# Kernel optimization log

Measured on AMD Instinct MI355X. Metric: run time of the kernel, lower is better.

Reference implementation:

```python
import jax, jax.numpy as jnp
import numpy as np

B, N, E, F, FE = 4, 10000, 160000, 128, 16  # batch, nodes, edges, filters(=node feat dim), edge feat dim
EPS = 1e-3  # keras LayerNormalization default epsilon


def layernorm(x, gamma, beta):
    mu = jnp.mean(x, axis=-1, keepdims=True)
    var = jnp.mean(jnp.square(x - mu), axis=-1, keepdims=True)
    return (x - mu) * jax.lax.rsqrt(var + EPS) * gamma + beta


def setup_inputs() -> dict:
    key = jax.random.key(0)
    ks = jax.random.split(key, 8)
    nodes = jax.random.normal(ks[0], (B, N, F), dtype=jnp.float32)
    edge_features = jax.random.normal(ks[1], (B, E, FE), dtype=jnp.float32)
    edges = jax.random.randint(ks[2], (B, E, 2), 0, N, dtype=jnp.int32)
    edge_weights = jax.random.uniform(ks[3], (B, E, 1), dtype=jnp.float32)
    edge_dropout = jnp.ones((B, E, 2), dtype=jnp.float32)
    W_msg = jax.random.normal(ks[4], (2 * F + FE, F), dtype=jnp.float32) * 0.02
    b_msg = jnp.zeros((F,), jnp.float32)
    g_msg = jnp.ones((F,), jnp.float32)
    beta_msg = jnp.zeros((F,), jnp.float32)
    W_upd = jax.random.normal(ks[5], (2 * F, F), dtype=jnp.float32) * 0.02
    b_upd = jnp.zeros((F,), jnp.float32)
    g_upd = jnp.ones((F,), jnp.float32)
    beta_upd = jnp.zeros((F,), jnp.float32)
    return dict(nodes=nodes, edge_features=edge_features, edges=edges,
                edge_weights=edge_weights, edge_dropout=edge_dropout,
                W_msg=W_msg, b_msg=b_msg, g_msg=g_msg, beta_msg=beta_msg,
                W_upd=W_upd, b_upd=b_upd, g_upd=g_upd, beta_upd=beta_upd)


def reference(nodes, edge_features, edges, edge_weights, edge_dropout,
              W_msg, b_msg, g_msg, beta_msg, W_upd, b_upd, g_upd, beta_upd):
    n = nodes.shape[1]
    # gather both endpoints per edge: [B,E,2,F] -> [B,E,2F]
    gathered = jax.vmap(lambda nd, ed: nd[ed])(nodes, edges)
    msg_in = gathered.reshape(gathered.shape[0], gathered.shape[1], -1)
    msg_in = jnp.concatenate([msg_in, edge_features], axis=-1)
    # message MLP: Dense + GELU + LayerNorm
    h = jnp.einsum('bei,io->beo', msg_in, W_msg) + b_msg
    messages = layernorm(jax.nn.gelu(h, approximate=False), g_msg, beta_msg)
    weighted_messages = messages * edge_weights
    # scatter-sum to destination nodes (edge[:,1]), masked by dropout col 1
    dropped = weighted_messages * edge_dropout[..., 1:2]
    dst = edges[..., 1]
    aggregated = jax.vmap(lambda m, d: jax.ops.segment_sum(m, d, num_segments=n))(dropped, dst)
    # update: concat + Dense + GELU + LayerNorm
    combined = jnp.concatenate([nodes, aggregated], axis=-1)
    u = jnp.einsum('bni,io->bno', combined, W_upd) + b_upd
    updated_nodes = layernorm(jax.nn.gelu(u, approximate=False), g_upd, beta_upd)
    return updated_nodes
```

## Files before the change

### kernel.cpp

```cpp
#include <hip/hip_runtime.h>
#include <hip/hip_bf16.h>
#include <hip/hip_fp16.h>

#define BATCH   4
#define NNODES  10000
#define NEDGES  160000
#define FDIM    128
#define FEDIM   16
#define LNEPS   1e-3f

typedef __attribute__((ext_vector_type(8))) short v8s;
typedef __attribute__((ext_vector_type(4))) float v4f;

#define AGG_BYTES   ((size_t)BATCH * NNODES * FDIM * 2)
#define P_OFF       AGG_BYTES
#define P_BYTES     ((size_t)BATCH * NNODES * 256 * 2)
#define WTCAT_OFF   (P_OFF + P_BYTES)
#define WTUPD_OFF   (WTCAT_OFF + (size_t)256 * 128 * 2)
#define W3T_OFF     (WTUPD_OFF + (size_t)128 * 256 * 2)

static __device__ __forceinline__ unsigned short f2bf(float f) {
    __hip_bfloat16 h = __float2bfloat16(f);
    return *reinterpret_cast<unsigned short*>(&h);
}
static __device__ __forceinline__ float bfbits2f(unsigned bits16) {
    return __uint_as_float(bits16 << 16);
}

static __device__ __forceinline__ float gelu_f(float x) {
    float z = 0.7978845608028654f * (x + 0.044715f * x * x * x);
    float e = __expf(2.0f * z);
    float t = 1.0f - 2.0f / (e + 1.0f);
    return 0.5f * x * (1.0f + t);
}

static __device__ __forceinline__ bool is_bf16_mode(const void* gflag) {
    return ((*reinterpret_cast<const unsigned*>(gflag)) & 0xFFFFu) != 0u;
}
static __device__ __forceinline__ float ld_f(const void* p, long i, bool bf) {
    return bf ? (float)reinterpret_cast<const __hip_bfloat16*>(p)[i]
              : reinterpret_cast<const float*>(p)[i];
}
static __device__ __forceinline__ uint4 pack8(const float* p) {
    float4 f0 = *reinterpret_cast<const float4*>(p);
    float4 f1 = *reinterpret_cast<const float4*>(p + 4);
    uint4 o;
    o.x = f2bf(f0.x) | ((unsigned)f2bf(f0.y) << 16);
    o.y = f2bf(f0.z) | ((unsigned)f2bf(f0.w) << 16);
    o.z = f2bf(f1.x) | ((unsigned)f2bf(f1.y) << 16);
    o.w = f2bf(f1.z) | ((unsigned)f2bf(f1.w) << 16);
    return o;
}
static __device__ __forceinline__ uint4 h8_to_bf8(uint4 u) {
    unsigned w[4] = {u.x, u.y, u.z, u.w};
    uint4 o; unsigned r[4];
    #pragma unroll
    for (int q = 0; q < 4; q++) {
        __half lo = *reinterpret_cast<const __half*>(&w[q]);
        unsigned short hib = (unsigned short)(w[q] >> 16);
        __half hi = *reinterpret_cast<const __half*>(&hib);
        r[q] = f2bf(__half2float(lo)) | ((unsigned)f2bf(__half2float(hi)) << 16);
    }
    o.x = r[0]; o.y = r[1]; o.z = r[2]; o.w = r[3];
    return o;
}

#define NCAT (256 * 128)
#define NUPD (128 * 256)
#define NW3  (128 * 32)
__global__ void prep_weights(const void* __restrict__ Wmsg, const void* __restrict__ Wupd,
                             const void* __restrict__ gflag,
                             unsigned short* __restrict__ WtCat,
                             unsigned short* __restrict__ WtUpd,
                             unsigned short* __restrict__ W3t) {
    bool bf = is_bf16_mode(gflag);
    int i = blockIdx.x * 256 + threadIdx.x;
    if (i < NCAT) {
        int n = i >> 7, k = i & 127;
        int src = (n < 128) ? (k * 128 + n) : ((128 + k) * 128 + (n - 128));
        WtCat[i] = bf ? reinterpret_cast<const unsigned short*>(Wmsg)[src]
                      : f2bf(reinterpret_cast<const float*>(Wmsg)[src]);
    } else if (i < NCAT + NUPD) {
        int j = i - NCAT;
        int n = j >> 8, c = j & 255;
        WtUpd[j] = bf ? reinterpret_cast<const unsigned short*>(Wupd)[c * 128 + n]
                      : f2bf(reinterpret_cast<const float*>(Wupd)[c * 128 + n]);
    } else if (i < NCAT + NUPD + NW3) {
        int j = i - NCAT - NUPD;
        int n = j >> 5, k = j & 31;
        W3t[j] = (k < 16) ? (bf ? reinterpret_cast<const unsigned short*>(Wmsg)[(256 + k) * 128 + n]
                                : f2bf(reinterpret_cast<const float*>(Wmsg)[(256 + k) * 128 + n]))
                          : (unsigned short)0;
    }
}

__global__ __launch_bounds__(256) void pg_kernel(
    const void* __restrict__ nodes,
    const void* __restrict__ bmsg,
    const void* __restrict__ gflag,
    const unsigned short* __restrict__ Wt,
    unsigned short*       __restrict__ P)
{
    const bool bf = is_bf16_mode(gflag);
    __shared__ unsigned short sW[128 * 40];
    __shared__ unsigned short sA[128 * 40];

    const int tid  = threadIdx.x;
    const int lane = tid & 63, wave = tid >> 6;
    const int c    = lane & 15, quad = lane >> 4;
    const int row0 = blockIdx.x * 128;
    const int half = blockIdx.y;
    const int NROWS = BATCH * NNODES;

    float bcol[8];
    #pragma unroll
    for (int nt = 0; nt < 8; nt++)
        bcol[nt] = (half == 0) ? ld_f(bmsg, nt * 16 + c, bf) : 0.f;

    v4f acc[2][8];
    #pragma unroll
    for (int mt = 0; mt < 2; mt++)
        #pragma unroll
        for (int nt = 0; nt < 8; nt++) { v4f z = {0.f, 0.f, 0.f, 0.f}; acc[mt][nt] = z; }

    for (int ks = 0; ks < 4; ks++) {
        #pragma unroll
        for (int q = tid; q < 512; q += 256) {
            int n = q >> 2, part = q & 3;
            *reinterpret_cast<uint4*>(&sW[n * 40 + part * 8]) =
                *reinterpret_cast<const uint4*>(Wt + (half * 128 + n) * 128 + ks * 32 + part * 8);
        }
        #pragma unroll
        for (int q = tid; q < 512; q += 256) {
            int t = q >> 2, part = q & 3;
            int row = row0 + t; if (row >= NROWS) row = NROWS - 1;
            long off = (size_t)row * FDIM + ks * 32 + part * 8;
            uint4 v = bf ? *reinterpret_cast<const uint4*>(reinterpret_cast<const unsigned short*>(nodes) + off)
                         : pack8(reinterpret_cast<const float*>(nodes) + off);
            *reinterpret_cast<uint4*>(&sA[t * 40 + part * 8]) = v;
        }
        __syncthreads();

        v8s a0 = *reinterpret_cast<const v8s*>(&sA[(wave * 32 + c) * 40 + quad * 8]);
        v8s a1 = *reinterpret_cast<const v8s*>(&sA[(wave * 32 + 16 + c) * 40 + quad * 8]);
        #pragma unroll
        for (int nt = 0; nt < 8; nt++) {
            v8s bfr = *reinterpret_cast<const v8s*>(&sW[(nt * 16 + c) * 40 + quad * 8]);
            acc[0][nt] = __builtin_amdgcn_mfma_f32_16x16x32_bf16(a0, bfr, acc[0][nt], 0, 0, 0);
            acc[1][nt] = __builtin_amdgcn_mfma_f32_16x16x32_bf16(a1, bfr, acc[1][nt], 0, 0, 0);
        }
        __syncthreads();
    }

    #pragma unroll
    for (int mt = 0; mt < 2; mt++)
        #pragma unroll
        for (int r = 0; r < 4; r++) {
            int row = row0 + wave * 32 + mt * 16 + quad * 4 + r;
            if (row < NROWS) {
                float v[8];
                #pragma unroll
                for (int nt = 0; nt < 8; nt++) v[nt] = acc[mt][nt][r] + bcol[nt];
                uint4 o;
                o.x = f2bf(v[0]) | ((unsigned)f2bf(v[1]) << 16);
                o.y = f2bf(v[2]) | ((unsigned)f2bf(v[3]) << 16);
                o.z = f2bf(v[4]) | ((unsigned)f2bf(v[5]) << 16);
                o.w = f2bf(v[6]) | ((unsigned)f2bf(v[7]) << 16);
                *reinterpret_cast<uint4*>(P + (size_t)row * 256 + half * 128 + c * 8) = o;
            }
        }
}

__global__ __launch_bounds__(256) void edge_kernel(
    const unsigned short* __restrict__ P,
    const void* __restrict__ efeat,
    const int*  __restrict__ edges,
    const void* __restrict__ ew,
    const void* __restrict__ ed,
    const unsigned short* __restrict__ W3t,
    const void* __restrict__ gmsg,
    const void* __restrict__ betamsg,
    __half*     __restrict__ agg)
{
    const bool bf = is_bf16_mode(gmsg);
    __shared__ int   sSrc[128], sDst[128];
    __shared__ float sWgt[128];

    const int tid  = threadIdx.x;
    const int b    = blockIdx.x / (NEDGES / 128);
    const int e0   = (blockIdx.x % (NEDGES / 128)) * 128;
    const int lane = tid & 63, wave = tid >> 6;
    const int c    = lane & 15, quad = lane >> 4;

    if (tid < 128) {
        long be = (long)b * NEDGES + e0 + tid;
        sSrc[tid] = edges[be * 2];
        sDst[tid] = edges[be * 2 + 1];
        sWgt[tid] = ld_f(ew, be, bf) * ld_f(ed, be * 2 + 1, bf);
    }

    float gcol[8], becol[8];
    #pragma unroll
    for (int nt = 0; nt < 8; nt++) {
        gcol[nt]  = ld_f(gmsg, nt * 16 + c, bf);
        becol[nt] = ld_f(betamsg, nt * 16 + c, bf);
    }

    v8s bfrag[8];
    #pragma unroll
    for (int nt = 0; nt < 8; nt++)
        bfrag[nt] = *reinterpret_cast<const v8s*>(W3t + (nt * 16 + c) * 32 + quad * 8);

    v4f acc[2][8];
    #pragma unroll
    for (int mt = 0; mt < 2; mt++)
        #pragma unroll
        for (int nt = 0; nt < 8; nt++) { v4f z = {0.f, 0.f, 0.f, 0.f}; acc[mt][nt] = z; }

    #pragma unroll
    for (int mt = 0; mt < 2; mt++) {
        v8s a = {0, 0, 0, 0, 0, 0, 0, 0};
        if (quad < 2) {
            long ebase = ((long)b * NEDGES + e0 + wave * 32 + mt * 16 + c) * FEDIM + quad * 8;
            if (bf) {
                uint4 u = *reinterpret_cast<const uint4*>(reinterpret_cast<const unsigned short*>(efeat) + ebase);
                a = *reinterpret_cast<v8s*>(&u);
            } else {
                uint4 u = pack8(reinterpret_cast<const float*>(efeat) + ebase);
                a = *reinterpret_cast<v8s*>(&u);
            }
        }
        #pragma unroll
        for (int nt = 0; nt < 8; nt++)
            acc[mt][nt] = __builtin_amdgcn_mfma_f32_16x16x32_bf16(a, bfrag[nt], acc[mt][nt], 0, 0, 0);
    }

    __syncthreads();

    const size_t nbase = (size_t)b * NNODES;
    const bool even = !(c & 1);

    #pragma unroll
    for (int mt = 0; mt < 2; mt++) {
        uint4 U1[4], U2[4];
        #pragma unroll
        for (int r = 0; r < 4; r++) {
            int m = wave * 32 + mt * 16 + quad * 4 + r;
            U1[r] = *reinterpret_cast<const uint4*>(P + (nbase + sSrc[m]) * 256 + c * 8);
            U2[r] = *reinterpret_cast<const uint4*>(P + (nbase + sDst[m]) * 256 + 128 + c * 8);
        }
        #pragma unroll
        for (int r = 0; r < 4; r++) {
            int m = wave * 32 + mt * 16 + quad * 4 + r;
            unsigned w1[4] = {U1[r].x, U1[r].y, U1[r].z, U1[r].w};
            unsigned w2[4] = {U2[r].x, U2[r].y, U2[r].z, U2[r].w};
            float h[8];
            #pragma unroll
            for (int q = 0; q < 4; q++) {
                h[q * 2]     = bfbits2f(w1[q] & 0xFFFFu) + bfbits2f(w2[q] & 0xFFFFu) + acc[mt][q * 2][r];
                h[q * 2 + 1] = __uint_as_float(w1[q] & 0xFFFF0000u) + __uint_as_float(w2[q] & 0xFFFF0000u)
                               + acc[mt][q * 2 + 1][r];
            }
            float s = 0.f, sq = 0.f;
            #pragma unroll
            for (int nt = 0; nt < 8; nt++) {
                float g = gelu_f(h[nt]);
                h[nt] = g; s += g; sq += g * g;
            }
            #pragma unroll
            for (int off = 1; off < 16; off <<= 1) {
                s  += __shfl_xor(s, off);
                sq += __shfl_xor(sq, off);
            }
            float mu  = s * (1.0f / 128.0f);
            float var = sq * (1.0f / 128.0f) - mu * mu;
            float rs  = rsqrtf(var + LNEPS);
            float wgt = sWgt[m];
            float y[8];
            #pragma unroll
            for (int nt = 0; nt < 8; nt++)
                y[nt] = ((h[nt] - mu) * rs * gcol[nt] + becol[nt]) * wgt;

            __half* aout = agg + (nbase + sDst[m]) * FDIM;
            #pragma unroll
            for (int np = 0; np < 4; np++) {
                int nt = np * 2;
                float t0 = __shfl_xor(y[nt], 1);
                float t1 = __shfl_xor(y[nt + 1], 1);
                __half2 v = even ? __floats2half2_rn(y[nt], t0)
                                 : __floats2half2_rn(t1, y[nt + 1]);
                int hoff = even ? (nt * 16 + c) : ((nt + 1) * 16 + c - 1);
                unsafeAtomicAdd(reinterpret_cast<__half2*>(aout + hoff), v);
            }
        }
    }
}

__global__ __launch_bounds__(256) void upd_kernel(
    const void* __restrict__ nodes,
    const __half* __restrict__ agg,
    const unsigned short* __restrict__ Wt,
    const void* __restrict__ bupd,
    const void* __restrict__ gupd,
    const void* __restrict__ beupd,
    void*       __restrict__ out)
{
    const bool bf = is_bf16_mode(gupd);
    __shared__ unsigned short sW[128 * 40];
    __shared__ unsigned short sA[64 * 40];

    const int tid  = threadIdx.x;
    const int lane = tid & 63, wave = tid >> 6;
    const int c    = lane & 15, quad = lane >> 4;
    const int row0 = blockIdx.x * 64;

    float bcol[8], gcol[8], becol[8];
    #pragma unroll
    for (int nt = 0; nt < 8; nt++) {
        int col = nt * 16 + c;
        bcol[nt]  = ld_f(bupd, col, bf);
        gcol[nt]  = ld_f(gupd, col, bf);
        becol[nt] = ld_f(beupd, col, bf);
    }

    v4f acc[8];
    #pragma unroll
    for (int nt = 0; nt < 8; nt++) { v4f z = {0.f, 0.f, 0.f, 0.f}; acc[nt] = z; }

    for (int ks = 0; ks < 8; ks++) {
        #pragma unroll
        for (int q = tid; q < 512; q += 256) {
            int n = q >> 2, part = q & 3;
            *reinterpret_cast<uint4*>(&sW[n * 40 + part * 8]) =
                *reinterpret_cast<const uint4*>(Wt + n * 256 + ks * 32 + part * 8);
        }
        {
            int t = tid >> 2, part = tid & 3;
            int row = row0 + t;
            uint4 v;
            if (ks < 4) {
                long off = (size_t)row * FDIM + ks * 32 + part * 8;
                v = bf ? *reinterpret_cast<const uint4*>(reinterpret_cast<const unsigned short*>(nodes) + off)
                       : pack8(reinterpret_cast<const float*>(nodes) + off);
            } else {
                uint4 u = *reinterpret_cast<const uint4*>(
                    reinterpret_cast<const unsigned short*>(agg) + (size_t)row * FDIM + (ks - 4) * 32 + part * 8);
                v = h8_to_bf8(u);
            }
            *reinterpret_cast<uint4*>(&sA[t * 40 + part * 8]) = v;
        }
        __syncthreads();

        v8s a0 = *reinterpret_cast<const v8s*>(&sA[(wave * 16 + c) * 40 + quad * 8]);
        #pragma unroll
        for (int nt = 0; nt < 8; nt++) {
            v8s bfr = *reinterpret_cast<const v8s*>(&sW[(nt * 16 + c) * 40 + quad * 8]);
            acc[nt] = __builtin_amdgcn_mfma_f32_16x16x32_bf16(a0, bfr, acc[nt], 0, 0, 0);
        }
        __syncthreads();
    }

    float s[4] = {0, 0, 0, 0}, sq[4] = {0, 0, 0, 0};
    #pragma unroll
    for (int nt = 0; nt < 8; nt++) {
        v4f v = acc[nt];
        #pragma unroll
        for (int r = 0; r < 4; r++) {
            float g = gelu_f(v[r] + bcol[nt]);
            v[r] = g;
            s[r] += g; sq[r] += g * g;
        }
        acc[nt] = v;
    }
    #pragma unroll
    for (int off = 1; off < 16; off <<= 1) {
        #pragma unroll
        for (int r = 0; r < 4; r++) {
            s[r]  += __shfl_xor(s[r], off);
            sq[r] += __shfl_xor(sq[r], off);
        }
    }
    #pragma unroll
    for (int r = 0; r < 4; r++) {
        float mu  = s[r] * (1.0f / 128.0f);
        float var = sq[r] * (1.0f / 128.0f) - mu * mu;
        float rs  = rsqrtf(var + LNEPS);
        int row = row0 + wave * 16 + quad * 4 + r;
        #pragma unroll
        for (int nt = 0; nt < 8; nt++) {
            float y = (acc[nt][r] - mu) * rs * gcol[nt] + becol[nt];
            size_t oi = (size_t)row * FDIM + nt * 16 + c;
            if (bf) reinterpret_cast<__hip_bfloat16*>(out)[oi] = __float2bfloat16(y);
            else    reinterpret_cast<float*>(out)[oi] = y;
        }
    }
}

extern "C" void kernel_launch(void* const* d_in, const int* in_sizes, int n_in,
                              void* d_out, int out_size, void* d_ws, size_t ws_size,
                              hipStream_t stream)
{
    const void* nodes   = d_in[0];
    const void* efeat   = d_in[1];
    const int*  edges   = (const int*)d_in[2];
    const void* ew      = d_in[3];
    const void* ed      = d_in[4];
    const void* Wmsg    = d_in[5];
    const void* bmsg    = d_in[6];
    const void* gmsg    = d_in[7];
    const void* betamsg = d_in[8];
    const void* Wupd    = d_in[9];
    const void* bupd    = d_in[10];
    const void* gupd    = d_in[11];
    const void* betaupd = d_in[12];

    char* ws = (char*)d_ws;
    __half* agg = (__half*)ws;
    unsigned short* P     = (unsigned short*)(ws + P_OFF);
    unsigned short* WtCat = (unsigned short*)(ws + WTCAT_OFF);
    unsigned short* WtUpd = (unsigned short*)(ws + WTUPD_OFF);
    unsigned short* W3t   = (unsigned short*)(ws + W3T_OFF);

    hipMemsetAsync(agg, 0, AGG_BYTES, stream);
    prep_weights<<<(NCAT + NUPD + NW3 + 255) / 256, 256, 0, stream>>>(
        Wmsg, Wupd, gmsg, WtCat, WtUpd, W3t);
    pg_kernel<<<dim3((BATCH * NNODES + 127) / 128, 2), 256, 0, stream>>>(
        nodes, bmsg, gmsg, WtCat, P);
    edge_kernel<<<BATCH * (NEDGES / 128), 256, 0, stream>>>(
        P, efeat, edges, ew, ed, W3t, gmsg, betamsg, agg);
    upd_kernel<<<BATCH * NNODES / 64, 256, 0, stream>>>(
        nodes, agg, WtUpd, bupd, gupd, betaupd, d_out);
}
```

Measured before the change: 291.0 us.

## Split update GEMM: precompute node half in pg_kernel, fp16 MFMA on agg

```diff
diff --git a/kernel.cpp b/kernel.cpp
--- a/kernel.cpp
+++ b/kernel.cpp
@@ -8,23 +8,35 @@
 #define FDIM    128
 #define FEDIM   16
 #define LNEPS   1e-3f
-
-typedef __attribute__((ext_vector_type(8))) short v8s;
-typedef __attribute__((ext_vector_type(4))) float v4f;
-
-#define AGG_BYTES   ((size_t)BATCH * NNODES * FDIM * 2)
+#define NROWS   (BATCH * NNODES)
+
+typedef __attribute__((ext_vector_type(8))) short    v8s;
+typedef _Float16 v8h __attribute__((ext_vector_type(8)));
+typedef __attribute__((ext_vector_type(4))) float    v4f;
+
+#define AGG_BYTES   ((size_t)NROWS * FDIM * 2)
 #define P_OFF       AGG_BYTES
-#define P_BYTES     ((size_t)BATCH * NNODES * 256 * 2)
-#define WTCAT_OFF   (P_OFF + P_BYTES)
-#define WTUPD_OFF   (WTCAT_OFF + (size_t)256 * 128 * 2)
-#define W3T_OFF     (WTUPD_OFF + (size_t)128 * 256 * 2)
+#define P_BYTES     ((size_t)NROWS * 256 * 2)
+#define P3_OFF      (P_OFF + P_BYTES)
+#define P3_BYTES    ((size_t)NROWS * 128 * 2)
+#define WTCAT_OFF   (P3_OFF + P3_BYTES)
+#define W3T_OFF     (WTCAT_OFF + (size_t)384 * 128 * 2)
+#define WU2F_OFF    (W3T_OFF + (size_t)128 * 32 * 2)
 
 static __device__ __forceinline__ unsigned short f2bf(float f) {
     __hip_bfloat16 h = __float2bfloat16(f);
     return *reinterpret_cast<unsigned short*>(&h);
 }
+static __device__ __forceinline__ unsigned short f2h(float f) {
+    __half h = __float2half(f);
+    return *reinterpret_cast<unsigned short*>(&h);
+}
 static __device__ __forceinline__ float bfbits2f(unsigned bits16) {
     return __uint_as_float(bits16 << 16);
+}
+static __device__ __forceinline__ float hbits2f(unsigned short b) {
+    __half h = *reinterpret_cast<const __half*>(&b);
+    return __half2float(h);
 }
 
 static __device__ __forceinline__ float gelu_f(float x) {
@@ -51,55 +63,44 @@
     o.w = f2bf(f1.z) | ((unsigned)f2bf(f1.w) << 16);
     return o;
 }
-static __device__ __forceinline__ uint4 h8_to_bf8(uint4 u) {
-    unsigned w[4] = {u.x, u.y, u.z, u.w};
-    uint4 o; unsigned r[4];
-    #pragma unroll
-    for (int q = 0; q < 4; q++) {
-        __half lo = *reinterpret_cast<const __half*>(&w[q]);
-        unsigned short hib = (unsigned short)(w[q] >> 16);
-        __half hi = *reinterpret_cast<const __half*>(&hib);
-        r[q] = f2bf(__half2float(lo)) | ((unsigned)f2bf(__half2float(hi)) << 16);
-    }
-    o.x = r[0]; o.y = r[1]; o.z = r[2]; o.w = r[3];
-    return o;
-}
-
-#define NCAT (256 * 128)
-#define NUPD (128 * 256)
+
+#define NCAT (384 * 128)
 #define NW3  (128 * 32)
-__global__ void prep_weights(const void* __restrict__ Wmsg, const void* __restrict__ Wupd,
-                             const void* __restrict__ gflag,
-                             unsigned short* __restrict__ WtCat,
-                             unsigned short* __restrict__ WtUpd,
-                             unsigned short* __restrict__ W3t) {
+#define NU2  (128 * 128)
+#define NZERO ((int)(AGG_BYTES / 16))
+__global__ void prep_kernel(const void* __restrict__ Wmsg, const void* __restrict__ Wupd,
+                            const void* __restrict__ gflag,
+                            unsigned short* __restrict__ WtCat,
+                            unsigned short* __restrict__ W3t,
+                            unsigned short* __restrict__ Wu2f,
+                            uint4* __restrict__ aggz) {
     bool bf = is_bf16_mode(gflag);
     int i = blockIdx.x * 256 + threadIdx.x;
     if (i < NCAT) {
         int n = i >> 7, k = i & 127;
-        int src = (n < 128) ? (k * 128 + n) : ((128 + k) * 128 + (n - 128));
-        WtCat[i] = bf ? reinterpret_cast<const unsigned short*>(Wmsg)[src]
-                      : f2bf(reinterpret_cast<const float*>(Wmsg)[src]);
-    } else if (i < NCAT + NUPD) {
-        int j = i - NCAT;
-        int n = j >> 8, c = j & 255;
-        WtUpd[j] = bf ? reinterpret_cast<const unsigned short*>(Wupd)[c * 128 + n]
-                      : f2bf(reinterpret_cast<const float*>(Wupd)[c * 128 + n]);
-    } else if (i < NCAT + NUPD + NW3) {
-        int j = i - NCAT - NUPD;
-        int n = j >> 5, k = j & 31;
-        W3t[j] = (k < 16) ? (bf ? reinterpret_cast<const unsigned short*>(Wmsg)[(256 + k) * 128 + n]
-                                : f2bf(reinterpret_cast<const float*>(Wmsg)[(256 + k) * 128 + n]))
-                          : (unsigned short)0;
-    }
+        float v;
+        if (n < 128)      v = ld_f(Wmsg, (long)k * 128 + n, bf);
+        else if (n < 256) v = ld_f(Wmsg, (long)(128 + k) * 128 + (n - 128), bf);
+        else              v = ld_f(Wupd, (long)k * 128 + (n - 256), bf);
+        WtCat[i] = f2bf(v);
+    } else if (i < NCAT + NW3) {
+        int j = i - NCAT; int n = j >> 5, k = j & 31;
+        W3t[j] = (k < 16) ? f2bf(ld_f(Wmsg, (long)(256 + k) * 128 + n, bf)) : (unsigned short)0;
+    } else if (i < NCAT + NW3 + NU2) {
+        int j = i - NCAT - NW3; int n = j >> 7, k = j & 127;
+        Wu2f[j] = f2h(ld_f(Wupd, (long)(128 + k) * 128 + n, bf));
+    }
+    if (i < NZERO) aggz[i] = make_uint4(0u, 0u, 0u, 0u);
 }
 
 __global__ __launch_bounds__(256) void pg_kernel(
     const void* __restrict__ nodes,
     const void* __restrict__ bmsg,
+    const void* __restrict__ bupd,
     const void* __restrict__ gflag,
     const unsigned short* __restrict__ Wt,
-    unsigned short*       __restrict__ P)
+    unsigned short*       __restrict__ P,
+    unsigned short*       __restrict__ P3)
 {
     const bool bf = is_bf16_mode(gflag);
     __shared__ unsigned short sW[128 * 40];
@@ -110,12 +111,14 @@
     const int c    = lane & 15, quad = lane >> 4;
     const int row0 = blockIdx.x * 128;
     const int half = blockIdx.y;
-    const int NROWS = BATCH * NNODES;
 
     float bcol[8];
     #pragma unroll
-    for (int nt = 0; nt < 8; nt++)
-        bcol[nt] = (half == 0) ? ld_f(bmsg, nt * 16 + c, bf) : 0.f;
+    for (int nt = 0; nt < 8; nt++) {
+        if (half == 0)      bcol[nt] = ld_f(bmsg, nt * 16 + c, bf);
+        else if (half == 2) bcol[nt] = ld_f(bupd, nt * 16 + c, bf);
+        else                bcol[nt] = 0.f;
+    }
 
     v4f acc[2][8];
     #pragma unroll
@@ -162,11 +165,19 @@
                 #pragma unroll
                 for (int nt = 0; nt < 8; nt++) v[nt] = acc[mt][nt][r] + bcol[nt];
                 uint4 o;
-                o.x = f2bf(v[0]) | ((unsigned)f2bf(v[1]) << 16);
-                o.y = f2bf(v[2]) | ((unsigned)f2bf(v[3]) << 16);
-                o.z = f2bf(v[4]) | ((unsigned)f2bf(v[5]) << 16);
-                o.w = f2bf(v[6]) | ((unsigned)f2bf(v[7]) << 16);
-                *reinterpret_cast<uint4*>(P + (size_t)row * 256 + half * 128 + c * 8) = o;
+                if (half < 2) {
+                    o.x = f2bf(v[0]) | ((unsigned)f2bf(v[1]) << 16);
+                    o.y = f2bf(v[2]) | ((unsigned)f2bf(v[3]) << 16);
+                    o.z = f2bf(v[4]) | ((unsigned)f2bf(v[5]) << 16);
+                    o.w = f2bf(v[6]) | ((unsigned)f2bf(v[7]) << 16);
+                    *reinterpret_cast<uint4*>(P + (size_t)row * 256 + half * 128 + c * 8) = o;
+                } else {
+                    o.x = f2h(v[0]) | ((unsigned)f2h(v[1]) << 16);
+                    o.y = f2h(v[2]) | ((unsigned)f2h(v[3]) << 16);
+                    o.z = f2h(v[4]) | ((unsigned)f2h(v[5]) << 16);
+                    o.w = f2h(v[6]) | ((unsigned)f2h(v[7]) << 16);
+                    *reinterpret_cast<uint4*>(P3 + (size_t)row * 128 + c * 8) = o;
+                }
             }
         }
 }
@@ -297,103 +308,98 @@
 }
 
 __global__ __launch_bounds__(256) void upd_kernel(
-    const void* __restrict__ nodes,
     const __half* __restrict__ agg,
-    const unsigned short* __restrict__ Wt,
-    const void* __restrict__ bupd,
+    const unsigned short* __restrict__ P3,
+    const unsigned short* __restrict__ Wu2f,
     const void* __restrict__ gupd,
     const void* __restrict__ beupd,
     void*       __restrict__ out)
 {
     const bool bf = is_bf16_mode(gupd);
-    __shared__ unsigned short sW[128 * 40];
-    __shared__ unsigned short sA[64 * 40];
+    __shared__ unsigned short sW[128 * 136];
 
     const int tid  = threadIdx.x;
     const int lane = tid & 63, wave = tid >> 6;
     const int c    = lane & 15, quad = lane >> 4;
-    const int row0 = blockIdx.x * 64;
-
-    float bcol[8], gcol[8], becol[8];
+    const int row0 = blockIdx.x * 128;
+
+    for (int q = tid; q < 2048; q += 256) {
+        int n = q >> 4, part = q & 15;
+        *reinterpret_cast<uint4*>(&sW[n * 136 + part * 8]) =
+            *reinterpret_cast<const uint4*>(Wu2f + n * 128 + part * 8);
+    }
+
+    float gcol[8], becol[8];
     #pragma unroll
     for (int nt = 0; nt < 8; nt++) {
-        int col = nt * 16 + c;
-        bcol[nt]  = ld_f(bupd, col, bf);
-        gcol[nt]  = ld_f(gupd, col, bf);
-        becol[nt] = ld_f(beupd, col, bf);
-    }
-
-    v4f acc[8];
-    #pragma unroll
-    for (int nt = 0; nt < 8; nt++) { v4f z = {0.f, 0.f, 0.f, 0.f}; acc[nt] = z; }
-
-    for (int ks = 0; ks < 8; ks++) {
-        #pragma unroll
-        for (int q = tid; q < 512; q += 256) {
-            int n = q >> 2, part = q & 3;
-            *reinterpret_cast<uint4*>(&sW[n * 40 + part * 8]) =
-                *reinterpret_cast<const uint4*>(Wt + n * 256 + ks * 32 + part * 8);
-        }
-        {
-            int t = tid >> 2, part = tid & 3;
-            int row = row0 + t;
-            uint4 v;
-            if (ks < 4) {
-                long off = (size_t)row * FDIM + ks * 32 + part * 8;
-                v = bf ? *reinterpret_cast<const uint4*>(reinterpret_cast<const unsigned short*>(nodes) + off)
-                       : pack8(reinterpret_cast<const float*>(nodes) + off);
-            } else {
-                uint4 u = *reinterpret_cast<const uint4*>(
-                    reinterpret_cast<const unsigned short*>(agg) + (size_t)row * FDIM + (ks - 4) * 32 + part * 8);
-                v = h8_to_bf8(u);
-            }
-            *reinterpret_cast<uint4*>(&sA[t * 40 + part * 8]) = v;
-        }
-        __syncthreads();
-
-        v8s a0 = *reinterpret_cast<const v8s*>(&sA[(wave * 16 + c) * 40 + quad * 8]);
-        #pragma unroll
-        for (int nt = 0; nt < 8; nt++) {
-            v8s bfr = *reinterpret_cast<const v8s*>(&sW[(nt * 16 + c) * 40 + quad * 8]);
-            acc[nt] = __builtin_amdgcn_mfma_f32_16x16x32_bf16(a0, bfr, acc[nt], 0, 0, 0);
-        }
-        __syncthreads();
-    }
-
-    float s[4] = {0, 0, 0, 0}, sq[4] = {0, 0, 0, 0};
-    #pragma unroll
-    for (int nt = 0; nt < 8; nt++) {
-        v4f v = acc[nt];
+        gcol[nt]  = ld_f(gupd, nt * 16 + c, bf);
+        becol[nt] = ld_f(beupd, nt * 16 + c, bf);
+    }
+
+    v4f acc[2][8];
+    #pragma unroll
+    for (int mt = 0; mt < 2; mt++)
+        #pragma unroll
+        for (int nt = 0; nt < 8; nt++) { v4f z = {0.f, 0.f, 0.f, 0.f}; acc[mt][nt] = z; }
+
+    __syncthreads();
+
+    #pragma unroll
+    for (int ks = 0; ks < 4; ks++) {
+        v8h bfr[8];
+        #pragma unroll
+        for (int nt = 0; nt < 8; nt++)
+            bfr[nt] = *reinterpret_cast<const v8h*>(&sW[(nt * 16 + c) * 136 + ks * 32 + quad * 8]);
+        #pragma unroll
+        for (int mt = 0; mt < 2; mt++) {
+            int row = row0 + wave * 32 + mt * 16 + c; if (row >= NROWS) row = NROWS - 1;
+            v8h a = *reinterpret_cast<const v8h*>(
+                reinterpret_cast<const unsigned short*>(agg) + (size_t)row * FDIM + ks * 32 + quad * 8);
+            #pragma unroll
+            for (int nt = 0; nt < 8; nt++)
+                acc[mt][nt] = __builtin_amdgcn_mfma_f32_16x16x32_f16(a, bfr[nt], acc[mt][nt], 0, 0, 0);
+        }
+    }
+
+    #pragma unroll
+    for (int mt = 0; mt < 2; mt++)
         #pragma unroll
         for (int r = 0; r < 4; r++) {
-            float g = gelu_f(v[r] + bcol[nt]);
-            v[r] = g;
-            s[r] += g; sq[r] += g * g;
-        }
-        acc[nt] = v;
-    }
-    #pragma unroll
-    for (int off = 1; off < 16; off <<= 1) {
-        #pragma unroll
-        for (int r = 0; r < 4; r++) {
-            s[r]  += __shfl_xor(s[r], off);
-            sq[r] += __shfl_xor(sq[r], off);
-        }
-    }
-    #pragma unroll
-    for (int r = 0; r < 4; r++) {
-        float mu  = s[r] * (1.0f / 128.0f);
-        float var = sq[r] * (1.0f / 128.0f) - mu * mu;
-        float rs  = rsqrtf(var + LNEPS);
-        int row = row0 + wave * 16 + quad * 4 + r;
-        #pragma unroll
-        for (int nt = 0; nt < 8; nt++) {
-            float y = (acc[nt][r] - mu) * rs * gcol[nt] + becol[nt];
-            size_t oi = (size_t)row * FDIM + nt * 16 + c;
-            if (bf) reinterpret_cast<__hip_bfloat16*>(out)[oi] = __float2bfloat16(y);
-            else    reinterpret_cast<float*>(out)[oi] = y;
-        }
-    }
+            int row = row0 + wave * 32 + mt * 16 + quad * 4 + r;
+            bool valid = row < NROWS;
+            int rowc = valid ? row : NROWS - 1;
+            uint4 u = *reinterpret_cast<const uint4*>(P3 + (size_t)rowc * 128 + c * 8);
+            unsigned w[4] = {u.x, u.y, u.z, u.w};
+            float h[8];
+            #pragma unroll
+            for (int q = 0; q < 4; q++) {
+                h[q * 2]     = hbits2f((unsigned short)(w[q] & 0xFFFFu))  + acc[mt][q * 2][r];
+                h[q * 2 + 1] = hbits2f((unsigned short)(w[q] >> 16))      + acc[mt][q * 2 + 1][r];
+            }
+            float s = 0.f, sq = 0.f;
+            #pragma unroll
+            for (int nt = 0; nt < 8; nt++) {
+                float g = gelu_f(h[nt]);
+                h[nt] = g; s += g; sq += g * g;
+            }
+            #pragma unroll
+            for (int off = 1; off < 16; off <<= 1) {
+                s  += __shfl_xor(s, off);
+                sq += __shfl_xor(sq, off);
+            }
+            float mu  = s * (1.0f / 128.0f);
+            float var = sq * (1.0f / 128.0f) - mu * mu;
+            float rs  = rsqrtf(var + LNEPS);
+            if (valid) {
+                #pragma unroll
+                for (int nt = 0; nt < 8; nt++) {
+                    float y = (h[nt] - mu) * rs * gcol[nt] + becol[nt];
+                    size_t oi = (size_t)row * FDIM + nt * 16 + c;
+                    if (bf) reinterpret_cast<__hip_bfloat16*>(out)[oi] = __float2bfloat16(y);
+                    else    reinterpret_cast<float*>(out)[oi] = y;
+                }
+            }
+        }
 }
 
 extern "C" void kernel_launch(void* const* d_in, const int* in_sizes, int n_in,
@@ -417,17 +423,17 @@
     char* ws = (char*)d_ws;
     __half* agg = (__half*)ws;
     unsigned short* P     = (unsigned short*)(ws + P_OFF);
+    unsigned short* P3    = (unsigned short*)(ws + P3_OFF);
     unsigned short* WtCat = (unsigned short*)(ws + WTCAT_OFF);
-    unsigned short* WtUpd = (unsigned short*)(ws + WTUPD_OFF);
     unsigned short* W3t   = (unsigned short*)(ws + W3T_OFF);
-
-    hipMemsetAsync(agg, 0, AGG_BYTES, stream);
-    prep_weights<<<(NCAT + NUPD + NW3 + 255) / 256, 256, 0, stream>>>(
-        Wmsg, Wupd, gmsg, WtCat, WtUpd, W3t);
-    pg_kernel<<<dim3((BATCH * NNODES + 127) / 128, 2), 256, 0, stream>>>(
-        nodes, bmsg, gmsg, WtCat, P);
+    unsigned short* Wu2f  = (unsigned short*)(ws + WU2F_OFF);
+
+    prep_kernel<<<(NZERO + 255) / 256, 256, 0, stream>>>(
+        Wmsg, Wupd, gmsg, WtCat, W3t, Wu2f, (uint4*)agg);
+    pg_kernel<<<dim3((NROWS + 127) / 128, 3), 256, 0, stream>>>(
+        nodes, bmsg, bupd, gmsg, WtCat, P, P3);
     edge_kernel<<<BATCH * (NEDGES / 128), 256, 0, stream>>>(
         P, efeat, edges, ew, ed, W3t, gmsg, betamsg, agg);
-    upd_kernel<<<BATCH * NNODES / 64, 256, 0, stream>>>(
-        nodes, agg, WtUpd, bupd, gupd, betaupd, d_out);
-}
+    upd_kernel<<<(NROWS + 127) / 128, 256, 0, stream>>>(
+        agg, P3, Wu2f, gupd, betaupd, d_out);
+}
```

Result: no change. 294.2 us (+1.1%).
